# Kernel optimization log

Measured on AMD Instinct MI355X. Metric: run time of the kernel, lower is better.

Reference implementation:

```python
import jax, jax.numpy as jnp
import numpy as np

N = 33554432
MARGIN = 1.0


def setup_inputs() -> dict:
    key = jax.random.key(0)
    k1, k2 = jax.random.split(key)
    predictions = jax.random.normal(k1, (N,), dtype=jnp.float32)
    # labels in {-1, +1}
    labels = 2 * jax.random.randint(k2, (N,), 0, 2, dtype=jnp.int32) - 1
    return {"predictions": predictions, "labels": labels}


def reference(predictions, labels):
    # Original loop math:
    #   over positives: a += 1; b += 2*(margin - p_i); c += (margin - p_i)^2
    #   over negatives: loss += a*p_j^2 + b*p_j + c
    # Vectorized as masked reductions.
    dt = predictions.dtype
    pos = labels == 1
    neg = labels == -1
    z = jnp.where(pos, MARGIN - predictions, jnp.zeros((), dt))  # margin - p on positives
    a = jnp.sum(pos.astype(dt))
    b = 2.0 * jnp.sum(z)
    c = jnp.sum(z * z)
    pn = jnp.where(neg, predictions, jnp.zeros((), dt))
    n_neg = jnp.sum(neg.astype(dt))
    loss = a * jnp.sum(pn * pn) + b * jnp.sum(pn) + c * n_neg
    return loss
```

## Files before the change

kernel.cpp:

```cpp
#include <hip/hip_runtime.h>


constexpr float MARGIN = 1.0f;

#define BANK_STRIDE 32
#define BLOCK 256
#define GPT 8
#define GROUPS_PER_TILE (BLOCK * GPT)
#define PERSISTENT_BLOCKS 1024

struct Acc { float a, sz, sz2, sp, sp2; };

__device__ __forceinline__ float wave_reduce(float v) {
    #pragma unroll
    for (int off = 32; off > 0; off >>= 1) v += __shfl_down(v, off, 64);
    return v;
}

__device__ __forceinline__ void acc1(float px, int lx, Acc& s) {
    float ispos = (lx == 1) ? 1.0f : 0.0f;
    float z  = ispos * (MARGIN - px);
    s.a   += ispos;
    s.sz  += z;
    s.sz2  = fmaf(z, z, s.sz2);
    float pn = (lx == 1) ? 0.0f : px;
    s.sp  += pn;
    s.sp2  = fmaf(pn, pn, s.sp2);
}

__device__ __forceinline__ void load_batch(
    const float4* __restrict__ p4, const int4* __restrict__ l4,
    int tile, int tid, float4 (&pv)[GPT], int4 (&lv)[GPT])
{
    const int b = tile * GROUPS_PER_TILE + tid;
    #pragma unroll
    for (int k = 0; k < GPT; ++k) pv[k] = p4[b + k * BLOCK];
    #pragma unroll
    for (int k = 0; k < GPT; ++k) lv[k] = l4[b + k * BLOCK];
}

__device__ __forceinline__ void consume(
    const float4 (&pv)[GPT], const int4 (&lv)[GPT], Acc& s)
{
    #pragma unroll
    for (int k = 0; k < GPT; ++k) {
        acc1(pv[k].x, lv[k].x, s);
        acc1(pv[k].y, lv[k].y, s);
        acc1(pv[k].z, lv[k].z, s);
        acc1(pv[k].w, lv[k].w, s);
    }
}

__global__ __launch_bounds__(BLOCK, 2) void hinge2_reduce(
    const float* __restrict__ pred, const int* __restrict__ lab,
    float* __restrict__ ws, int nvec, int nfull, int nbanks, int bank_stride)
{
    const float4* p4 = reinterpret_cast<const float4*>(pred);
    const int4*   l4 = reinterpret_cast<const int4*>(lab);

    Acc s = {0.f, 0.f, 0.f, 0.f, 0.f};
    const int tid    = threadIdx.x;
    const int stride = gridDim.x;

    float4 pvA[GPT], pvB[GPT];
    int4   lvA[GPT], lvB[GPT];

    int t = blockIdx.x;
    if (t < nfull) {
        load_batch(p4, l4, t, tid, pvA, lvA);
        __builtin_amdgcn_sched_barrier(0);
        int tn = t + stride;
        while (tn < nfull) {
            load_batch(p4, l4, tn, tid, pvB, lvB);
            __builtin_amdgcn_sched_barrier(0);
            consume(pvA, lvA, s);
            tn += stride;
            if (tn >= nfull) { consume(pvB, lvB, s); goto tiles_done; }
            load_batch(p4, l4, tn, tid, pvA, lvA);
            __builtin_amdgcn_sched_barrier(0);
            consume(pvB, lvB, s);
            tn += stride;
        }
        consume(pvA, lvA, s);
tiles_done: ;
    }

    for (int i = nfull * GROUPS_PER_TILE + blockIdx.x * BLOCK + tid;
         i < nvec; i += stride * BLOCK) {
        float4 p = p4[i];
        int4   l = l4[i];
        acc1(p.x, l.x, s); acc1(p.y, l.y, s);
        acc1(p.z, l.z, s); acc1(p.w, l.w, s);
    }

    s.a   = wave_reduce(s.a);
    s.sz  = wave_reduce(s.sz);
    s.sz2 = wave_reduce(s.sz2);
    s.sp  = wave_reduce(s.sp);
    s.sp2 = wave_reduce(s.sp2);

    __shared__ float sdata[4][5];
    int lane = tid & 63;
    int wid  = tid >> 6;
    if (lane == 0) {
        sdata[wid][0] = s.a;
        sdata[wid][1] = s.sz;
        sdata[wid][2] = s.sz2;
        sdata[wid][3] = s.sp;
        sdata[wid][4] = s.sp2;
    }
    __syncthreads();

    if (tid == 0) {
        float t0 = 0.f, t1 = 0.f, t2 = 0.f, t3 = 0.f, t4 = 0.f;
        #pragma unroll
        for (int w = 0; w < 4; ++w) {
            t0 += sdata[w][0];
            t1 += sdata[w][1];
            t2 += sdata[w][2];
            t3 += sdata[w][3];
            t4 += sdata[w][4];
        }
        float* bank = ws + (blockIdx.x & (nbanks - 1)) * bank_stride;
        atomicAdd(&bank[0], t0);
        atomicAdd(&bank[1], t1);
        atomicAdd(&bank[2], t2);
        atomicAdd(&bank[3], t3);
        atomicAdd(&bank[4], t4);
    }
}

__global__ __launch_bounds__(256) void hinge2_final(
    const float* __restrict__ ws,
    const float* __restrict__ pred, const int* __restrict__ lab,
    float* __restrict__ out, int n, int tail_start,
    int nbanks, int bank_stride)
{
    int t = threadIdx.x;
    float a = 0.f, sz = 0.f, sz2 = 0.f, sp = 0.f, sp2 = 0.f;
    for (int b = t; b < nbanks; b += 256) {
        const float* bank = ws + b * bank_stride;
        a   += bank[0];
        sz  += bank[1];
        sz2 += bank[2];
        sp  += bank[3];
        sp2 += bank[4];
    }
    a   = wave_reduce(a);
    sz  = wave_reduce(sz);
    sz2 = wave_reduce(sz2);
    sp  = wave_reduce(sp);
    sp2 = wave_reduce(sp2);

    __shared__ float sdata[4][5];
    int lane = t & 63, wid = t >> 6;
    if (lane == 0) {
        sdata[wid][0] = a;  sdata[wid][1] = sz; sdata[wid][2] = sz2;
        sdata[wid][3] = sp; sdata[wid][4] = sp2;
    }
    __syncthreads();

    if (t == 0) {
        double A = 0, SZ = 0, SZ2 = 0, SP = 0, SP2 = 0;
        #pragma unroll
        for (int w = 0; w < 4; ++w) {
            A   += sdata[w][0];
            SZ  += sdata[w][1];
            SZ2 += sdata[w][2];
            SP  += sdata[w][3];
            SP2 += sdata[w][4];
        }
        for (int i = tail_start; i < n; ++i) {
            float p = pred[i];
            if (lab[i] == 1) {
                double z = (double)MARGIN - (double)p;
                A += 1.0; SZ += z; SZ2 += z * z;
            } else {
                SP += (double)p; SP2 += (double)p * (double)p;
            }
        }
        double loss = A * SP2 + 2.0 * SZ * SP + SZ2 * ((double)n - A);
        out[0] = (float)loss;
    }
}

extern "C" void kernel_launch(void* const* d_in, const int* in_sizes, int n_in,
                              void* d_out, int out_size, void* d_ws, size_t ws_size,
                              hipStream_t stream)
{
    const float* pred = (const float*)d_in[0];
    const int*   lab  = (const int*)d_in[1];
    float*       out  = (float*)d_out;
    float*       ws   = (float*)d_ws;

    int n    = in_sizes[0];
    int nvec = n >> 2;
    int tail = nvec << 2;
    int nfull = nvec / GROUPS_PER_TILE;

    int bank_stride = BANK_STRIDE;
    size_t max_banks = ws_size / (bank_stride * sizeof(float));
    int nbanks = 1;
    if (max_banks == 0) { bank_stride = 5; nbanks = 1; }
    else { while (nbanks * 2 <= (int)max_banks && nbanks < 256) nbanks <<= 1; }

    hipMemsetAsync(ws, 0, (size_t)nbanks * bank_stride * sizeof(float), stream);

    int blocks = nfull < PERSISTENT_BLOCKS ? nfull : PERSISTENT_BLOCKS;
    if (blocks < 1) blocks = 1;
    hinge2_reduce<<<blocks, BLOCK, 0, stream>>>(pred, lab, ws, nvec, nfull,
                                                nbanks, bank_stride);
    hinge2_final<<<1, BLOCK, 0, stream>>>(ws, pred, lab, out, n, tail,
                                          nbanks, bank_stride);
}
```

Before: 277.1 us.

## Replace double-buffered persistent tiles with simple grid-stride loop and per-block slots

Drops the register double-buffered tile pipeline (8 float4+int4 per thread per batch) in favour of a plain grid-stride loop that loads two float4/int4 pairs per iteration. It raises occupancy (launch bounds 8, up to 2048 blocks) so latency is hidden by more waves instead of explicit prefetch. Per-block partials go to dedicated slots instead of atomics, which removes the memset launch, and the final kernel sums them in double. The risk is that fewer bytes in flight per thread may lower achieved bandwidth, and it depends on the workspace holding enough slots.

```diff
diff --git a/kernel.cpp b/kernel.cpp
--- a/kernel.cpp
+++ b/kernel.cpp
@@ -3,19 +3,17 @@
 
 constexpr float MARGIN = 1.0f;
 
-#define BANK_STRIDE 32
 #define BLOCK 256
-#define GPT 8
-#define GROUPS_PER_TILE (BLOCK * GPT)
-#define PERSISTENT_BLOCKS 1024
-
-struct Acc { float a, sz, sz2, sp, sp2; };
+#define MAX_BLOCKS 2048
+#define SLOT_STRIDE 8
 
 __device__ __forceinline__ float wave_reduce(float v) {
     #pragma unroll
     for (int off = 32; off > 0; off >>= 1) v += __shfl_down(v, off, 64);
     return v;
 }
+
+struct Acc { float a, sz, sz2, sp, sp2; };
 
 __device__ __forceinline__ void acc1(float px, int lx, Acc& s) {
     float ispos = (lx == 1) ? 1.0f : 0.0f;
@@ -28,69 +26,38 @@
     s.sp2  = fmaf(pn, pn, s.sp2);
 }
 
-__device__ __forceinline__ void load_batch(
-    const float4* __restrict__ p4, const int4* __restrict__ l4,
-    int tile, int tid, float4 (&pv)[GPT], int4 (&lv)[GPT])
-{
-    const int b = tile * GROUPS_PER_TILE + tid;
-    #pragma unroll
-    for (int k = 0; k < GPT; ++k) pv[k] = p4[b + k * BLOCK];
-    #pragma unroll
-    for (int k = 0; k < GPT; ++k) lv[k] = l4[b + k * BLOCK];
+__device__ __forceinline__ void acc4(const float4& p, const int4& l, Acc& s) {
+    acc1(p.x, l.x, s);
+    acc1(p.y, l.y, s);
+    acc1(p.z, l.z, s);
+    acc1(p.w, l.w, s);
 }
 
-__device__ __forceinline__ void consume(
-    const float4 (&pv)[GPT], const int4 (&lv)[GPT], Acc& s)
-{
-    #pragma unroll
-    for (int k = 0; k < GPT; ++k) {
-        acc1(pv[k].x, lv[k].x, s);
-        acc1(pv[k].y, lv[k].y, s);
-        acc1(pv[k].z, lv[k].z, s);
-        acc1(pv[k].w, lv[k].w, s);
-    }
-}
-
-__global__ __launch_bounds__(BLOCK, 2) void hinge2_reduce(
+__global__ __launch_bounds__(BLOCK, 8) void hinge2_reduce(
     const float* __restrict__ pred, const int* __restrict__ lab,
-    float* __restrict__ ws, int nvec, int nfull, int nbanks, int bank_stride)
+    float* __restrict__ ws, int nvec)
 {
     const float4* p4 = reinterpret_cast<const float4*>(pred);
     const int4*   l4 = reinterpret_cast<const int4*>(lab);
 
     Acc s = {0.f, 0.f, 0.f, 0.f, 0.f};
-    const int tid    = threadIdx.x;
-    const int stride = gridDim.x;
+    const int tid  = threadIdx.x;
+    const int step = gridDim.x * (BLOCK * 2);
+    int i = blockIdx.x * (BLOCK * 2) + tid;
 
-    float4 pvA[GPT], pvB[GPT];
-    int4   lvA[GPT], lvB[GPT];
-
-    int t = blockIdx.x;
-    if (t < nfull) {
-        load_batch(p4, l4, t, tid, pvA, lvA);
-        __builtin_amdgcn_sched_barrier(0);
-        int tn = t + stride;
-        while (tn < nfull) {
-            load_batch(p4, l4, tn, tid, pvB, lvB);
-            __builtin_amdgcn_sched_barrier(0);
-            consume(pvA, lvA, s);
-            tn += stride;
-            if (tn >= nfull) { consume(pvB, lvB, s); goto tiles_done; }
-            load_batch(p4, l4, tn, tid, pvA, lvA);
-            __builtin_amdgcn_sched_barrier(0);
-            consume(pvB, lvB, s);
-            tn += stride;
-        }
-        consume(pvA, lvA, s);
-tiles_done: ;
+    while (i + BLOCK < nvec) {
+        float4 p0 = p4[i];
+        float4 p1 = p4[i + BLOCK];
+        int4   l0 = l4[i];
+        int4   l1 = l4[i + BLOCK];
+        acc4(p0, l0, s);
+        acc4(p1, l1, s);
+        i += step;
     }
-
-    for (int i = nfull * GROUPS_PER_TILE + blockIdx.x * BLOCK + tid;
-         i < nvec; i += stride * BLOCK) {
+    if (i < nvec) {
         float4 p = p4[i];
         int4   l = l4[i];
-        acc1(p.x, l.x, s); acc1(p.y, l.y, s);
-        acc1(p.z, l.z, s); acc1(p.w, l.w, s);
+        acc4(p, l, s);
     }
 
     s.a   = wave_reduce(s.a);
@@ -121,38 +88,40 @@
             t3 += sdata[w][3];
             t4 += sdata[w][4];
         }
-        float* bank = ws + (blockIdx.x & (nbanks - 1)) * bank_stride;
-        atomicAdd(&bank[0], t0);
-        atomicAdd(&bank[1], t1);
-        atomicAdd(&bank[2], t2);
-        atomicAdd(&bank[3], t3);
-        atomicAdd(&bank[4], t4);
+        float* slot = ws + (size_t)blockIdx.x * SLOT_STRIDE;
+        slot[0] = t0;
+        slot[1] = t1;
+        slot[2] = t2;
+        slot[3] = t3;
+        slot[4] = t4;
     }
 }
 
-__global__ __launch_bounds__(256) void hinge2_final(
+__global__ __launch_bounds__(BLOCK) void hinge2_final(
     const float* __restrict__ ws,
     const float* __restrict__ pred, const int* __restrict__ lab,
-    float* __restrict__ out, int n, int tail_start,
-    int nbanks, int bank_stride)
+    float* __restrict__ out, int n, int tail_start, int nslots)
 {
     int t = threadIdx.x;
-    float a = 0.f, sz = 0.f, sz2 = 0.f, sp = 0.f, sp2 = 0.f;
-    for (int b = t; b < nbanks; b += 256) {
-        const float* bank = ws + b * bank_stride;
-        a   += bank[0];
-        sz  += bank[1];
-        sz2 += bank[2];
-        sp  += bank[3];
-        sp2 += bank[4];
+    double a = 0., sz = 0., sz2 = 0., sp = 0., sp2 = 0.;
+    for (int b = t; b < nslots; b += BLOCK) {
+        const float* slot = ws + (size_t)b * SLOT_STRIDE;
+        a   += (double)slot[0];
+        sz  += (double)slot[1];
+        sz2 += (double)slot[2];
+        sp  += (double)slot[3];
+        sp2 += (double)slot[4];
     }
-    a   = wave_reduce(a);
-    sz  = wave_reduce(sz);
-    sz2 = wave_reduce(sz2);
-    sp  = wave_reduce(sp);
-    sp2 = wave_reduce(sp2);
+    #pragma unroll
+    for (int off = 32; off > 0; off >>= 1) {
+        a   += __shfl_down(a,   off, 64);
+        sz  += __shfl_down(sz,  off, 64);
+        sz2 += __shfl_down(sz2, off, 64);
+        sp  += __shfl_down(sp,  off, 64);
+        sp2 += __shfl_down(sp2, off, 64);
+    }
 
-    __shared__ float sdata[4][5];
+    __shared__ double sdata[4][5];
     int lane = t & 63, wid = t >> 6;
     if (lane == 0) {
         sdata[wid][0] = a;  sdata[wid][1] = sz; sdata[wid][2] = sz2;
@@ -196,20 +165,14 @@
     int n    = in_sizes[0];
     int nvec = n >> 2;
     int tail = nvec << 2;
-    int nfull = nvec / GROUPS_PER_TILE;
 
-    int bank_stride = BANK_STRIDE;
-    size_t max_banks = ws_size / (bank_stride * sizeof(float));
-    int nbanks = 1;
-    if (max_banks == 0) { bank_stride = 5; nbanks = 1; }
-    else { while (nbanks * 2 <= (int)max_banks && nbanks < 256) nbanks <<= 1; }
+    int blocks = MAX_BLOCKS;
+    int needed = (nvec + BLOCK * 2 - 1) / (BLOCK * 2);
+    if (blocks > needed) blocks = needed;
+    size_t max_slots = ws_size / (SLOT_STRIDE * sizeof(float));
+    if (max_slots > 0 && (size_t)blocks > max_slots) blocks = (int)max_slots;
+    if (blocks < 1) blocks = 1;
 
-    hipMemsetAsync(ws, 0, (size_t)nbanks * bank_stride * sizeof(float), stream);
-
-    int blocks = nfull < PERSISTENT_BLOCKS ? nfull : PERSISTENT_BLOCKS;
-    if (blocks < 1) blocks = 1;
-    hinge2_reduce<<<blocks, BLOCK, 0, stream>>>(pred, lab, ws, nvec, nfull,
-                                                nbanks, bank_stride);
-    hinge2_final<<<1, BLOCK, 0, stream>>>(ws, pred, lab, out, n, tail,
-                                          nbanks, bank_stride);
+    hinge2_reduce<<<blocks, BLOCK, 0, stream>>>(pred, lab, ws, nvec);
+    hinge2_final<<<1, BLOCK, 0, stream>>>(ws, pred, lab, out, n, tail, blocks);
 }
```

Measured after the change: 276.5 us. Within noise of the previous version (-0.2%).
